# Performance work log

Hardware: AMD Instinct MI355X
Metric: run time of the kernel (lower is better)

The kernel has to match this reference:

```python
import jax, jax.numpy as jnp
import numpy as np

B, T, S, H = 32, 1, 4096, 1024

def setup_inputs() -> dict:
    key = jax.random.key(0)
    ks = jax.random.split(key, 8)
    query = jax.random.normal(ks[0], (B, T, H), dtype=jnp.float32)
    encoder_outputs = jax.random.normal(ks[1], (B, S, H), dtype=jnp.float32)
    src_lengths = jax.random.randint(ks[2], (B,), 1, S + 1, dtype=jnp.int64)
    sc = 1.0 / np.sqrt(H)
    Ws_w = jax.random.normal(ks[3], (H, H), dtype=jnp.float32) * sc   # torch Linear weight (out,in)
    Wh_w = jax.random.normal(ks[4], (H, H), dtype=jnp.float32) * sc
    v_w = jax.random.normal(ks[5], (1, H), dtype=jnp.float32) * sc
    Wout_w = jax.random.normal(ks[6], (H, 2 * H), dtype=jnp.float32) * sc
    return {"query": query, "encoder_outputs": encoder_outputs, "src_lengths": src_lengths,
            "Ws_w": Ws_w, "Wh_w": Wh_w, "v_w": v_w, "Wout_w": Wout_w}

def reference(query, encoder_outputs, src_lengths, Ws_w, Wh_w, v_w, Wout_w):
    # score(h, s) = v^T tanh(Ws q + Wh h); query is a single decoder step (T=1)
    q_proj = jnp.einsum('bth,oh->bto', query, Ws_w)            # (B,1,H)
    h_proj = jnp.einsum('bsh,oh->bso', encoder_outputs, Wh_w)  # (B,S,H)
    scores = jnp.einsum('bsh,h->bs', jnp.tanh(q_proj + h_proj), v_w[0])  # (B,S)
    # NOTE: original calls non-in-place masked_fill and discards the result,
    # so src_lengths has no effect on the output (replicated faithfully).
    attn = jax.nn.softmax(scores, axis=-1)                     # (B,S)
    ctx = jnp.einsum('bs,bsh->bh', attn, encoder_outputs)[:, None, :]  # (B,1,H)
    cat = jnp.concatenate([ctx, query], axis=-1)               # (B,1,2H)
    return jnp.tanh(jnp.einsum('btk,ok->bto', cat, Wout_w))    # (B,1,H)
```

## Files before the change

### kernel.cpp

```cpp
#include <hip/hip_runtime.h>
#include <hip/hip_bf16.h>

#define B_  32
#define S_  4096
#define H_  1024
#define M_  (B_*S_)

typedef __attribute__((ext_vector_type(8))) short bf16x8;
typedef __attribute__((ext_vector_type(4))) float f32x4;
typedef __attribute__((ext_vector_type(8))) unsigned short ushort8;

typedef void __attribute__((address_space(3)))* lds_ptr_t;
typedef void __attribute__((address_space(1)))* gbl_ptr_t;

__device__ __forceinline__ unsigned short f2bf(float x) {
    return __builtin_bit_cast(unsigned short, __float2bfloat16(x));
}
__device__ __forceinline__ float bf2f(unsigned short u) {
    return __builtin_bit_cast(float, (unsigned)u << 16);
}
__device__ __forceinline__ float tanh_fast(float x) {
    float e = __expf(2.0f * x);
    return 1.0f - 2.0f / (e + 1.0f);
}

__global__ __launch_bounds__(256) void k_cvt_bf16(const float* __restrict__ in,
                                                  unsigned short* __restrict__ out, int n4) {
    int i = blockIdx.x * 256 + threadIdx.x;
    if (i < n4) {
        float4 f = reinterpret_cast<const float4*>(in)[i];
        ushort4 u;
        u.x = f2bf(f.x); u.y = f2bf(f.y); u.z = f2bf(f.z); u.w = f2bf(f.w);
        reinterpret_cast<ushort4*>(out)[i] = u;
    }
}

__global__ __launch_bounds__(256) void k_cvt_enc(const float* __restrict__ in,
                                                 unsigned short* __restrict__ out, int n8) {
    const int stride = gridDim.x * 256;
    for (int i = blockIdx.x * 256 + threadIdx.x; i < n8; i += stride) {
        float4 a = reinterpret_cast<const float4*>(in)[(size_t)i * 2];
        float4 b = reinterpret_cast<const float4*>(in)[(size_t)i * 2 + 1];
        ushort8 u;
        u[0] = f2bf(a.x); u[1] = f2bf(a.y); u[2] = f2bf(a.z); u[3] = f2bf(a.w);
        u[4] = f2bf(b.x); u[5] = f2bf(b.y); u[6] = f2bf(b.z); u[7] = f2bf(b.w);
        reinterpret_cast<ushort8*>(out)[i] = u;
    }
}

__global__ __launch_bounds__(256) void k_qproj(const float* __restrict__ q,
                                               const float* __restrict__ Ws,
                                               float* __restrict__ qp) {
    const int b = blockIdx.y, oc = blockIdx.x, tid = threadIdx.x;
    __shared__ float ql[H_];
    for (int i = tid; i < H_; i += 256) ql[i] = q[b*H_ + i];
    __syncthreads();
    const int o = oc*256 + tid;
    const float4* w = reinterpret_cast<const float4*>(&Ws[(size_t)o * H_]);
    float acc = 0.f;
    #pragma unroll 4
    for (int k4 = 0; k4 < H_/4; ++k4) {
        float4 ww = w[k4];
        acc += ql[k4*4+0]*ww.x + ql[k4*4+1]*ww.y + ql[k4*4+2]*ww.z + ql[k4*4+3]*ww.w;
    }
    qp[b*H_ + o] = acc;
}

__global__ __launch_bounds__(512, 2) void k_scores8(const unsigned short* __restrict__ encb,
                                                    const unsigned short* __restrict__ whb,
                                                    const float* __restrict__ qp,
                                                    const float* __restrict__ vw,
                                                    float* __restrict__ sp) {
    __shared__ __align__(1024) char smem[131072];

    const int tid = threadIdx.x;
    const int l   = tid & 63;
    const int w   = tid >> 6;
    const int wr  = w >> 2;
    const int wc  = w & 3;
    const int fr  = l & 15;
    const int fh  = l >> 4;

    const int hb = blockIdx.x;
    const int L  = (hb & 7) * 256 + (hb >> 3);
    const int bm = L >> 2;
    const int bn = L & 3;
    const int row0 = bm * 256;
    const int col0 = bn * 256;
    const int b = row0 >> 12;

    const int g_roff = fr;
    const int g_koff = fh * 8;

    auto stageA = [&](int t, int mh) {
        #pragma unroll
        for (int j = 0; j < 2; ++j) {
            int s_local = j*8 + w;
            int g  = s_local >> 1;
            int kh = s_local & 1;
            int rblk = mh*4 + (g & 3) + ((g >> 2) << 3);
            const unsigned short* src = encb + (size_t)(row0 + rblk*16 + g_roff) * H_
                                             + t*64 + kh*32 + g_koff;
            char* dst = smem + (t & 1)*65536 + (rblk*2 + kh)*1024 + l*16;
            __builtin_amdgcn_global_load_lds((gbl_ptr_t)src, (lds_ptr_t)dst, 16, 0, 0);
        }
    };
    auto stageB = [&](int t, int q) {
        #pragma unroll
        for (int j = 0; j < 2; ++j) {
            int s_local = j*8 + w;
            int a2 = s_local >> 2;
            int b2 = (s_local >> 1) & 1;
            int kh = s_local & 1;
            int nblk = a2*4 + q*2 + b2;
            const unsigned short* src = whb + (size_t)(col0 + nblk*16 + g_roff) * H_
                                            + t*64 + kh*32 + g_koff;
            char* dst = smem + (t & 1)*65536 + 32768 + (nblk*2 + kh)*1024 + l*16;
            __builtin_amdgcn_global_load_lds((gbl_ptr_t)src, (lds_ptr_t)dst, 16, 0, 0);
        }
    };

    f32x4  acc[8][4] = {};
    bf16x8 af[4][2];
    bf16x8 ba[4][2];

    auto ldA = [&](int buf, int mq) {
        #pragma unroll
        for (int m2 = 0; m2 < 4; ++m2)
            #pragma unroll
            for (int kh = 0; kh < 2; ++kh) {
                int rblk = wr*8 + mq*4 + m2;
                af[m2][kh] = *reinterpret_cast<const bf16x8*>(
                    smem + buf*65536 + (rblk*2 + kh)*1024 + l*16);
            }
    };
    auto ldB = [&](int buf, int nq) {
        #pragma unroll
        for (int n2 = 0; n2 < 2; ++n2)
            #pragma unroll
            for (int kh = 0; kh < 2; ++kh) {
                int nblk = wc*4 + nq*2 + n2;
                ba[nq*2 + n2][kh] = *reinterpret_cast<const bf16x8*>(
                    smem + buf*65536 + 32768 + (nblk*2 + kh)*1024 + l*16);
            }
    };
    auto mfma16 = [&](int mq, int nq) {
        __builtin_amdgcn_s_setprio(1);
        #pragma unroll
        for (int kh = 0; kh < 2; ++kh)
            #pragma unroll
            for (int m2 = 0; m2 < 4; ++m2)
                #pragma unroll
                for (int n2 = 0; n2 < 2; ++n2)
                    acc[mq*4+m2][nq*2+n2] = __builtin_amdgcn_mfma_f32_16x16x32_bf16(
                        af[m2][kh], ba[nq*2+n2][kh], acc[mq*4+m2][nq*2+n2], 0, 0, 0);
        __builtin_amdgcn_s_setprio(0);
    };

    auto tile = [&](int t, bool s1, bool s2, bool last) {
        const int buf = t & 1;
        ldA(buf, 0); ldB(buf, 0);
        if (s1) stageA(t+1, 1);
        __builtin_amdgcn_s_barrier();
        asm volatile("s_waitcnt lgkmcnt(0)" ::: "memory");
        mfma16(0, 0);
        __builtin_amdgcn_s_barrier();
        ldB(buf, 1);
        if (s2) stageA(t+2, 0);
        __builtin_amdgcn_s_barrier();
        asm volatile("s_waitcnt lgkmcnt(0)" ::: "memory");
        mfma16(0, 1);
        __builtin_amdgcn_s_barrier();
        ldA(buf, 1);
        if (s2) stageB(t+2, 0);
        __builtin_amdgcn_s_barrier();
        asm volatile("s_waitcnt lgkmcnt(0)" ::: "memory");
        mfma16(1, 0);
        __builtin_amdgcn_s_barrier();
        if (s2) stageB(t+2, 1);
        __builtin_amdgcn_s_barrier();
        asm volatile("s_waitcnt lgkmcnt(0)" ::: "memory");
        mfma16(1, 1);
        if (!last) asm volatile("s_waitcnt vmcnt(6)" ::: "memory");
        else       asm volatile("s_waitcnt vmcnt(0)" ::: "memory");
        __builtin_amdgcn_s_barrier();
    };

    stageA(0, 0); stageB(0, 0); stageB(0, 1); stageA(0, 1);
    stageA(1, 0); stageB(1, 0); stageB(1, 1);
    asm volatile("s_waitcnt vmcnt(6)" ::: "memory");
    __builtin_amdgcn_s_barrier();

    for (int t = 0; t < 14; ++t) tile(t, true, true, false);
    tile(14, true,  false, true);
    tile(15, false, false, true);

    float vv[4], qq[4];
    #pragma unroll
    for (int n = 0; n < 4; ++n) {
        int c = col0 + wc*64 + n*16 + fr;
        vv[n] = vw[c];
        qq[n] = qp[b*H_ + c];
    }
    float* sred = (float*)smem;
    #pragma unroll
    for (int m = 0; m < 8; ++m)
        #pragma unroll
        for (int r = 0; r < 4; ++r) {
            float s = 0.f;
            #pragma unroll
            for (int n = 0; n < 4; ++n)
                s += vv[n] * tanh_fast(qq[n] + acc[m][n][r]);
            s += __shfl_xor(s, 1, 64); s += __shfl_xor(s, 2, 64);
            s += __shfl_xor(s, 4, 64); s += __shfl_xor(s, 8, 64);
            if (fr == 0) sred[wc*256 + wr*128 + m*16 + fh*4 + r] = s;
        }
    __syncthreads();
    if (tid < 256) {
        float s = sred[tid] + sred[256 + tid] + sred[512 + tid] + sred[768 + tid];
        sp[(size_t)bn * M_ + row0 + tid] = s;
    }
}

__global__ __launch_bounds__(256) void k_scores_f(const float* __restrict__ enc,
                                                  const unsigned short* __restrict__ whb,
                                                  const float* __restrict__ qp,
                                                  const float* __restrict__ vw,
                                                  float* __restrict__ sp) {
    __shared__ __align__(16) unsigned short As[2][128][32];
    __shared__ __align__(16) unsigned short Bs[2][128][32];
    __shared__ float sred[2][128];

    const int tid  = threadIdx.x;
    const int lane = tid & 63;
    const int wid  = tid >> 6;
    const int wr = wid >> 1, wc = wid & 1;
    const int fr = lane & 15;
    const int fk = (lane >> 4) * 8;

    const int h  = blockIdx.x;
    const int L  = (h & 7) * 1024 + (h >> 3);
    const int bm = L >> 3;
    const int bn = L & 7;
    const int row0 = bm * 128;
    const int col0 = bn * 128;
    const int b = row0 >> 12;

    const int ar = tid >> 3;
    const int ak = (tid & 7) * 4;
    const int bnr = tid >> 2;
    const int bkk = (tid & 3) * 8;

    float4 areg[4];
    auto loadA = [&](int kt) {
        #pragma unroll
        for (int p = 0; p < 4; ++p)
            areg[p] = *reinterpret_cast<const float4*>(
                &enc[(size_t)(row0 + p*32 + ar) * H_ + kt*32 + ak]);
    };
    auto writeA = [&](int buf) {
        #pragma unroll
        for (int p = 0; p < 4; ++p) {
            ushort4 u;
            u.x = f2bf(areg[p].x); u.y = f2bf(areg[p].y);
            u.z = f2bf(areg[p].z); u.w = f2bf(areg[p].w);
            *reinterpret_cast<ushort4*>(&As[buf][p*32 + ar][ak]) = u;
        }
    };
    auto stageB = [&](int buf, int kt) {
        const unsigned short* g0 = whb + (size_t)(col0 + bnr) * H_ + kt*32 + bkk;
        const unsigned short* g1 = g0 + (size_t)64 * H_;
        char* l0 = (char*)(&Bs[buf][0][0]) + tid*16;
        __builtin_amdgcn_global_load_lds((gbl_ptr_t)g0, (lds_ptr_t)l0,        16, 0, 0);
        __builtin_amdgcn_global_load_lds((gbl_ptr_t)g1, (lds_ptr_t)(l0+4096), 16, 0, 0);
    };

    f32x4 acc[4][4] = {};

    loadA(0);
    stageB(0, 0);
    writeA(0);
    __syncthreads();

    for (int kt = 0; kt < 32; ++kt) {
        const int cur = kt & 1, nxt = cur ^ 1;
        if (kt < 31) { stageB(nxt, kt + 1); loadA(kt + 1); }

        bf16x8 af[4], bfr[4];
        #pragma unroll
        for (int i = 0; i < 4; ++i) {
            af[i]  = *reinterpret_cast<const bf16x8*>(&As[cur][wr*64 + i*16 + fr][fk]);
            bfr[i] = *reinterpret_cast<const bf16x8*>(&Bs[cur][wc*64 + i*16 + fr][fk]);
        }
        #pragma unroll
        for (int i = 0; i < 4; ++i)
            #pragma unroll
            for (int j = 0; j < 4; ++j)
                acc[i][j] = __builtin_amdgcn_mfma_f32_16x16x32_bf16(af[i], bfr[j], acc[i][j], 0, 0, 0);

        if (kt < 31) writeA(nxt);
        __syncthreads();
    }

    float vv[4], qq[4];
    #pragma unroll
    for (int j = 0; j < 4; ++j) {
        int c = col0 + wc*64 + j*16 + fr;
        vv[j] = vw[c];
        qq[j] = qp[b*H_ + c];
    }
    #pragma unroll
    for (int i = 0; i < 4; ++i) {
        #pragma unroll
        for (int r = 0; r < 4; ++r) {
            float s = 0.f;
            #pragma unroll
            for (int j = 0; j < 4; ++j)
                s += vv[j] * tanh_fast(qq[j] + acc[i][j][r]);
            #pragma unroll
            for (int m = 1; m < 16; m <<= 1)
                s += __shfl_xor(s, m, 64);
            if (fr == 0)
                sred[wc][wr*64 + i*16 + (lane >> 4)*4 + r] = s;
        }
    }
    __syncthreads();
    if (tid < 128)
        sp[(size_t)bn * M_ + row0 + tid] = sred[0][tid] + sred[1][tid];
}

__global__ __launch_bounds__(256) void k_softmax(const float* __restrict__ sp,
                                                 float* __restrict__ attn, int P) {
    const int b = blockIdx.x, tid = threadIdx.x;
    __shared__ float red[4];
    float vals[16];
    float mx = -1e30f;
    #pragma unroll
    for (int i = 0; i < 16; ++i) {
        int s = i*256 + tid;
        float x = 0.f;
        for (int p = 0; p < P; ++p) x += sp[(size_t)p*M_ + b*S_ + s];
        vals[i] = x;
        mx = fmaxf(mx, x);
    }
    #pragma unroll
    for (int m = 1; m < 64; m <<= 1) mx = fmaxf(mx, __shfl_xor(mx, m, 64));
    if ((tid & 63) == 0) red[tid >> 6] = mx;
    __syncthreads();
    mx = fmaxf(fmaxf(red[0], red[1]), fmaxf(red[2], red[3]));
    float sum = 0.f;
    #pragma unroll
    for (int i = 0; i < 16; ++i) { vals[i] = __expf(vals[i] - mx); sum += vals[i]; }
    #pragma unroll
    for (int m = 1; m < 64; m <<= 1) sum += __shfl_xor(sum, m, 64);
    __syncthreads();
    if ((tid & 63) == 0) red[tid >> 6] = sum;
    __syncthreads();
    sum = red[0] + red[1] + red[2] + red[3];
    float inv = 1.f / sum;
    #pragma unroll
    for (int i = 0; i < 16; ++i) attn[b*S_ + i*256 + tid] = vals[i] * inv;
}

__global__ __launch_bounds__(256) void k_ctx_b(const float* __restrict__ attn,
                                               const unsigned short* __restrict__ encb,
                                               float* __restrict__ ctxp) {
    const int sc = blockIdx.x;
    const int b  = blockIdx.y;
    const int hh = threadIdx.x * 4;
    float ax = 0.f, ay = 0.f, az = 0.f, aw = 0.f;
    const int s0 = sc * 256;
    #pragma unroll 4
    for (int s = s0; s < s0 + 256; ++s) {
        float a = attn[b*S_ + s];
        ushort4 e = *reinterpret_cast<const ushort4*>(&encb[((size_t)b*S_ + s) * H_ + hh]);
        ax += a*bf2f(e.x); ay += a*bf2f(e.y); az += a*bf2f(e.z); aw += a*bf2f(e.w);
    }
    float4 o; o.x = ax; o.y = ay; o.z = az; o.w = aw;
    *reinterpret_cast<float4*>(&ctxp[((size_t)sc*B_ + b) * H_ + hh]) = o;
}

__global__ __launch_bounds__(256) void k_ctx_f(const float* __restrict__ attn,
                                               const float* __restrict__ enc,
                                               float* __restrict__ ctxp) {
    const int sc = blockIdx.x;
    const int b  = blockIdx.y;
    const int hh = threadIdx.x * 4;
    float ax = 0.f, ay = 0.f, az = 0.f, aw = 0.f;
    const int s0 = sc * 256;
    #pragma unroll 4
    for (int s = s0; s < s0 + 256; ++s) {
        float a = attn[b*S_ + s];
        float4 e = *reinterpret_cast<const float4*>(&enc[((size_t)b*S_ + s) * H_ + hh]);
        ax += a*e.x; ay += a*e.y; az += a*e.z; aw += a*e.w;
    }
    float4 o; o.x = ax; o.y = ay; o.z = az; o.w = aw;
    *reinterpret_cast<float4*>(&ctxp[((size_t)sc*B_ + b) * H_ + hh]) = o;
}

__global__ __launch_bounds__(256) void k_out(const float* __restrict__ ctxp,
                                             const float* __restrict__ q,
                                             const float* __restrict__ Wout,
                                             float* __restrict__ out) {
    const int oc = blockIdx.x, b = blockIdx.y, tid = threadIdx.x;
    __shared__ float cat[2*H_];
    for (int k = tid; k < H_; k += 256) {
        float s = 0.f;
        #pragma unroll
        for (int p = 0; p < 16; ++p) s += ctxp[((size_t)p*B_ + b) * H_ + k];
        cat[k] = s;
        cat[H_ + k] = q[b*H_ + k];
    }
    __syncthreads();
    const int o = oc*256 + tid;
    const float4* w = reinterpret_cast<const float4*>(&Wout[(size_t)o * 2*H_]);
    float acc = 0.f;
    #pragma unroll 4
    for (int k4 = 0; k4 < 2*H_/4; ++k4) {
        float4 ww = w[k4];
        acc += cat[k4*4+0]*ww.x + cat[k4*4+1]*ww.y + cat[k4*4+2]*ww.z + cat[k4*4+3]*ww.w;
    }
    out[b*H_ + o] = tanh_fast(acc);
}

extern "C" void kernel_launch(void* const* d_in, const int* in_sizes, int n_in,
                              void* d_out, int out_size, void* d_ws, size_t ws_size,
                              hipStream_t stream) {
    const float* query = (const float*)d_in[0];
    const float* enc   = (const float*)d_in[1];
    const float* Ws    = (const float*)d_in[3];
    const float* Wh    = (const float*)d_in[4];
    const float* vw    = (const float*)d_in[5];
    const float* Wout  = (const float*)d_in[6];
    float* out = (float*)d_out;

    char* ws = (char*)d_ws;

    if (ws_size >= (266ull << 20)) {
        unsigned short* encb = (unsigned short*)ws;
        unsigned short* whb  = (unsigned short*)(ws + (256ull << 20));
        float* sp   = (float*)(ws + (258ull << 20));
        float* attn = (float*)(ws + (262ull << 20));
        float* qp   = (float*)(ws + (262ull << 20) + (512u << 10));
        float* ctxp = (float*)(ws + (263ull << 20));

        k_cvt_enc <<<dim3(2048),    dim3(256), 0, stream>>>(enc, encb, M_*H_/8);
        k_cvt_bf16<<<dim3(1024),    dim3(256), 0, stream>>>(Wh, whb, H_*H_/4);
        k_qproj   <<<dim3(4, 32),   dim3(256), 0, stream>>>(query, Ws, qp);
        k_scores8 <<<dim3(2048),    dim3(512), 0, stream>>>(encb, whb, qp, vw, sp);
        k_softmax <<<dim3(32),      dim3(256), 0, stream>>>(sp, attn, 4);
        k_ctx_b   <<<dim3(16, 32),  dim3(256), 0, stream>>>(attn, encb, ctxp);
        k_out     <<<dim3(4, 32),   dim3(256), 0, stream>>>(ctxp, query, Wout, out);
    } else {
        unsigned short* whb = (unsigned short*)ws;
        float* sp   = (float*)(ws + (2u  << 20));
        float* attn = (float*)(ws + (6u  << 20));
        float* qp   = (float*)(ws + (6u  << 20) + (512u << 10));
        float* ctxp = (float*)(ws + (7u  << 20));

        k_cvt_bf16<<<dim3(1024),    dim3(256), 0, stream>>>(Wh, whb, H_*H_/4);
        k_qproj   <<<dim3(4, 32),   dim3(256), 0, stream>>>(query, Ws, qp);
        k_scores_f<<<dim3(8192),    dim3(256), 0, stream>>>(enc, whb, qp, vw, sp);
        k_softmax <<<dim3(32),      dim3(256), 0, stream>>>(sp, attn, 8);
        k_ctx_f   <<<dim3(16, 32),  dim3(256), 0, stream>>>(attn, enc, ctxp);
        k_out     <<<dim3(4, 32),   dim3(256), 0, stream>>>(ctxp, query, Wout, out);
    }
}
```

Baseline: 665.5 us.

## Precompute staging addresses, halve barriers per sub-tile, fully unroll K loop

Precomputes the global source and LDS destination offsets for the async global-to-LDS loads once, outside the K loop, and simplifies the LDS fragment offsets. The barrier+lgkmcnt(0) pair before each MFMA group is removed, leaving one raw s_barrier between groups, and the 16-step K loop is fully unrolled. The aim is less address arithmetic and fewer synchronisation stalls in the main GEMM. Without the explicit lgkmcnt wait before the MFMAs, ordering of LDS reads against stage writes relies on the compiler's waitcnt insertion and the remaining barriers, which risks races or extra register pressure from the unroll.

Measured after the change: 658.9 us. No clear change (-1.0%).

```diff
diff --git a/kernel.cpp b/kernel.cpp
--- a/kernel.cpp
+++ b/kernel.cpp
@@ -92,33 +92,47 @@
     const int g_roff = fr;
     const int g_koff = fh * 8;
 
-    auto stageA = [&](int t, int mh) {
+    const unsigned short* srcA[2][2];
+    const unsigned short* srcB[2][2];
+    int dstA[2][2], dstB[2][2];
+    {
         #pragma unroll
         for (int j = 0; j < 2; ++j) {
-            int s_local = j*8 + w;
-            int g  = s_local >> 1;
-            int kh = s_local & 1;
-            int rblk = mh*4 + (g & 3) + ((g >> 2) << 3);
-            const unsigned short* src = encb + (size_t)(row0 + rblk*16 + g_roff) * H_
-                                             + t*64 + kh*32 + g_koff;
-            char* dst = smem + (t & 1)*65536 + (rblk*2 + kh)*1024 + l*16;
-            __builtin_amdgcn_global_load_lds((gbl_ptr_t)src, (lds_ptr_t)dst, 16, 0, 0);
+            const int s_local = j*8 + w;
+            const int g  = s_local >> 1;
+            const int kh = s_local & 1;
+            const int a2 = s_local >> 2;
+            const int b2 = (s_local >> 1) & 1;
+            #pragma unroll
+            for (int mh = 0; mh < 2; ++mh) {
+                const int rblk = mh*4 + (g & 3) + ((g >> 2) << 3);
+                srcA[mh][j] = encb + (size_t)(row0 + rblk*16 + g_roff) * H_ + kh*32 + g_koff;
+                dstA[mh][j] = (rblk*2 + kh)*1024 + l*16;
+            }
+            #pragma unroll
+            for (int q = 0; q < 2; ++q) {
+                const int nblk = a2*4 + q*2 + b2;
+                srcB[q][j] = whb + (size_t)(col0 + nblk*16 + g_roff) * H_ + kh*32 + g_koff;
+                dstB[q][j] = 32768 + (nblk*2 + kh)*1024 + l*16;
+            }
         }
-    };
-    auto stageB = [&](int t, int q) {
-        #pragma unroll
-        for (int j = 0; j < 2; ++j) {
-            int s_local = j*8 + w;
-            int a2 = s_local >> 2;
-            int b2 = (s_local >> 1) & 1;
-            int kh = s_local & 1;
-            int nblk = a2*4 + q*2 + b2;
-            const unsigned short* src = whb + (size_t)(col0 + nblk*16 + g_roff) * H_
-                                            + t*64 + kh*32 + g_koff;
-            char* dst = smem + (t & 1)*65536 + 32768 + (nblk*2 + kh)*1024 + l*16;
-            __builtin_amdgcn_global_load_lds((gbl_ptr_t)src, (lds_ptr_t)dst, 16, 0, 0);
-        }
-    };
+    }
+
+    auto stA = [&](int t, int mh) {
+        #pragma unroll
+        for (int j = 0; j < 2; ++j)
+            __builtin_amdgcn_global_load_lds((gbl_ptr_t)(srcA[mh][j] + t*64),
+                (lds_ptr_t)(smem + ((t & 1) << 16) + dstA[mh][j]), 16, 0, 0);
+    };
+    auto stB = [&](int t, int q) {
+        #pragma unroll
+        for (int j = 0; j < 2; ++j)
+            __builtin_amdgcn_global_load_lds((gbl_ptr_t)(srcB[q][j] + t*64),
+                (lds_ptr_t)(smem + ((t & 1) << 16) + dstB[q][j]), 16, 0, 0);
+    };
+
+    const int aOffBase = wr*8*2048 + l*16;
+    const int bOffBase = 32768 + wc*4*2048 + l*16;
 
     f32x4  acc[8][4] = {};
     bf16x8 af[4][2];
@@ -128,21 +142,17 @@
         #pragma unroll
         for (int m2 = 0; m2 < 4; ++m2)
             #pragma unroll
-            for (int kh = 0; kh < 2; ++kh) {
-                int rblk = wr*8 + mq*4 + m2;
+            for (int kh = 0; kh < 2; ++kh)
                 af[m2][kh] = *reinterpret_cast<const bf16x8*>(
-                    smem + buf*65536 + (rblk*2 + kh)*1024 + l*16);
-            }
+                    smem + (buf << 16) + aOffBase + (mq*4 + m2)*2048 + kh*1024);
     };
     auto ldB = [&](int buf, int nq) {
         #pragma unroll
         for (int n2 = 0; n2 < 2; ++n2)
             #pragma unroll
-            for (int kh = 0; kh < 2; ++kh) {
-                int nblk = wc*4 + nq*2 + n2;
+            for (int kh = 0; kh < 2; ++kh)
                 ba[nq*2 + n2][kh] = *reinterpret_cast<const bf16x8*>(
-                    smem + buf*65536 + 32768 + (nblk*2 + kh)*1024 + l*16);
-            }
+                    smem + (buf << 16) + bOffBase + (nq*2 + n2)*2048 + kh*1024);
     };
     auto mfma16 = [&](int mq, int nq) {
         __builtin_amdgcn_s_setprio(1);
@@ -156,44 +166,37 @@
                         af[m2][kh], ba[nq*2+n2][kh], acc[mq*4+m2][nq*2+n2], 0, 0, 0);
         __builtin_amdgcn_s_setprio(0);
     };
+    auto barrier = [] { asm volatile("s_barrier" ::: "memory"); };
 
     auto tile = [&](int t, bool s1, bool s2, bool last) {
         const int buf = t & 1;
         ldA(buf, 0); ldB(buf, 0);
-        if (s1) stageA(t+1, 1);
-        __builtin_amdgcn_s_barrier();
-        asm volatile("s_waitcnt lgkmcnt(0)" ::: "memory");
+        if (s1) stA(t+1, 1);
         mfma16(0, 0);
-        __builtin_amdgcn_s_barrier();
+        barrier();
         ldB(buf, 1);
-        if (s2) stageA(t+2, 0);
-        __builtin_amdgcn_s_barrier();
-        asm volatile("s_waitcnt lgkmcnt(0)" ::: "memory");
+        if (s2) stA(t+2, 0);
         mfma16(0, 1);
-        __builtin_amdgcn_s_barrier();
+        barrier();
         ldA(buf, 1);
-        if (s2) stageB(t+2, 0);
-        __builtin_amdgcn_s_barrier();
-        asm volatile("s_waitcnt lgkmcnt(0)" ::: "memory");
+        if (s2) stB(t+2, 0);
         mfma16(1, 0);
-        __builtin_amdgcn_s_barrier();
-        if (s2) stageB(t+2, 1);
-        __builtin_amdgcn_s_barrier();
-        asm volatile("s_waitcnt lgkmcnt(0)" ::: "memory");
+        barrier();
+        if (s2) stB(t+2, 1);
         mfma16(1, 1);
         if (!last) asm volatile("s_waitcnt vmcnt(6)" ::: "memory");
         else       asm volatile("s_waitcnt vmcnt(0)" ::: "memory");
-        __builtin_amdgcn_s_barrier();
-    };
-
-    stageA(0, 0); stageB(0, 0); stageB(0, 1); stageA(0, 1);
-    stageA(1, 0); stageB(1, 0); stageB(1, 1);
+        barrier();
+    };
+
+    stA(0, 0); stB(0, 0); stB(0, 1); stA(0, 1);
+    stA(1, 0); stB(1, 0); stB(1, 1);
     asm volatile("s_waitcnt vmcnt(6)" ::: "memory");
-    __builtin_amdgcn_s_barrier();
-
-    for (int t = 0; t < 14; ++t) tile(t, true, true, false);
-    tile(14, true,  false, true);
-    tile(15, false, false, true);
+    barrier();
+
+    #pragma unroll
+    for (int t = 0; t < 16; ++t)
+        tile(t, t < 15, t < 14, t >= 14);
 
     float vv[4], qq[4];
     #pragma unroll
```
